# Kernel optimization log

Hardware: AMD Instinct MI355X
Metric: run time of the kernel (lower is better)

Reference implementation:

```python
import jax, jax.numpy as jnp
import numpy as np

B, IN, OUT = 2048, 64, 2048


def setup_inputs() -> dict:
    key = jax.random.key(0)
    k1, k2, k3 = jax.random.split(key, 3)
    x = jax.random.normal(k1, (B, IN), dtype=jnp.float32)
    # learned params (shapes per init: means [in, out], inv_std_dev [out, in, in])
    means = jax.random.uniform(k2, (IN, OUT), dtype=jnp.float32)
    # roughly like the inverse of a diagonal step matrix plus small noise
    inv_std_dev = (jax.random.normal(k3, (OUT, IN, IN), dtype=jnp.float32) * 0.05
                   + jnp.eye(IN, dtype=jnp.float32) * 0.5)
    return {"x": x, "means": means, "inv_std_dev": inv_std_dev}


def reference(x, means, inv_std_dev):
    # diff[b, o, i] = x[b, i] - means[i, o]   -> [B, OUT, IN]
    d = x[:, None, :] - means.T[None, :, :]
    # torch uses inv_std_dev.pow(2) (elementwise square), not a matrix square
    A = inv_std_dev * inv_std_dev  # [OUT, IN, IN]
    # per-neuron quadratic form: q[b, o] = d[b,o,:] @ A[o] @ d[b,o,:]
    q = jnp.einsum('boi,oij,boj->bo', d, A, d)
    return jnp.exp(-0.5 * q)  # [B, OUT]
```

## Files before the change

### kernel.cpp

```cpp
#include <hip/hip_runtime.h>
#include <hip/hip_bf16.h>

typedef __bf16 bf16x8 __attribute__((ext_vector_type(8)));
typedef float f32x4 __attribute__((ext_vector_type(4)));
typedef float f32x16 __attribute__((ext_vector_type(16)));

#define B_N 2048
#define O_N 2048
#define K_N 64

__device__ __forceinline__ void gld16(const void* g, void* l) {
    __builtin_amdgcn_global_load_lds(
        (const __attribute__((address_space(1))) void*)g,
        (__attribute__((address_space(3))) void*)l,
        16, 0, 0);
}

__global__ __launch_bounds__(256) void rbf_prep(
    const float* __restrict__ inv, const float* __restrict__ means,
    __bf16* __restrict__ Atp, __bf16* __restrict__ cPhi,
    __bf16* __restrict__ cPlo, float* __restrict__ kArr)
{
    __shared__ float s[64 * 65];
    __shared__ float mld[64];
    __shared__ float uw[128];
    const int o = blockIdx.x;
    const int t = threadIdx.x;
    const float4* src = (const float4*)(inv + (size_t)o * 4096);
#pragma unroll
    for (int k = 0; k < 4; ++k) {
        const int idx = k * 256 + t;
        const float4 v = src[idx];
        const int i = idx >> 4;
        const int j0 = (idx & 15) * 4;
        s[i * 65 + j0 + 0] = v.x * v.x;
        s[i * 65 + j0 + 1] = v.y * v.y;
        s[i * 65 + j0 + 2] = v.z * v.z;
        s[i * 65 + j0 + 3] = v.w * v.w;
    }
    if (t < 64) mld[t] = means[(size_t)t * O_N + o];
    __syncthreads();
    if (t < 64) {
        float u = 0.f;
#pragma unroll
        for (int i = 0; i < 64; ++i) u = fmaf(s[i * 65 + t], mld[i], u);
        uw[t] = u;
    } else if (t < 128) {
        const int j = t - 64;
        float w = 0.f;
#pragma unroll
        for (int i = 0; i < 64; ++i) w = fmaf(s[j * 65 + i], mld[i], w);
        uw[64 + j] = w;
    }
    __syncthreads();
    if (t < 64) {
        const float c = -(uw[t] + uw[64 + t]);
        const __bf16 hi = (__bf16)c;
        const __bf16 lo = (__bf16)(c - (float)hi);
        const size_t eidx = (size_t)(o >> 5) * 2048 + (size_t)(t >> 4) * 512
                          + (size_t)(o & 31) * 16 + (t & 15);
        cPhi[eidx] = hi;
        cPlo[eidx] = lo;
    }
    if (t == 0) {
        float kk = 0.f;
#pragma unroll
        for (int j = 0; j < 64; ++j) kk = fmaf(uw[j], mld[j], kk);
        kArr[o] = kk;
    }
#pragma unroll
    for (int r = 0; r < 2; ++r) {
        const int ch = r * 256 + t;
        const int ss = ch >> 7;
        const int j = (ch >> 1) & 63;
        const int hh = ch & 1;
        bf16x8 v;
#pragma unroll
        for (int e = 0; e < 8; ++e)
            v[e] = (__bf16)s[(16 * ss + 8 * hh + e) * 65 + j];
        *(bf16x8*)(Atp + (size_t)o * 4096 + (size_t)ch * 8) = v;
    }
}

__global__ __launch_bounds__(256, 2) void rbf_main(
    const float* __restrict__ x, const __bf16* __restrict__ Atp,
    const __bf16* __restrict__ cPhi, const __bf16* __restrict__ cPlo,
    const float* __restrict__ kArr, float* __restrict__ out)
{
    __shared__ __align__(16) __bf16 sA[3][4096];
    __shared__ __align__(16) float sLin[4][32][64];
    __shared__ float sK[32];

    const int tid = threadIdx.x;
    const int wave = tid >> 6;
    const int lane = tid & 63;
    const int b = lane & 31;
    const int h = lane >> 5;

    const int wg = (int)blockIdx.x;
    const int xcd = wg & 7;
    const int loc = wg >> 3;
    const int og = xcd * 8 + (loc >> 3);
    const int bg = loc & 7;
    const int oBase = og * 32;
    const int rowW = bg * 256 + wave * 64;

    const float* xr0 = x + (size_t)(rowW + b) * K_N;
    const float* xr1 = x + (size_t)(rowW + 32 + b) * K_N;

    const f32x16 zz = {0.f,0.f,0.f,0.f,0.f,0.f,0.f,0.f,
                       0.f,0.f,0.f,0.f,0.f,0.f,0.f,0.f};

    bf16x8 xh[2][4];
    f32x4 xd[2][2][4];
    {
        bf16x8 xl[2][4];
#pragma unroll
        for (int t = 0; t < 2; ++t) {
            const float* xr = t ? xr1 : xr0;
#pragma unroll
            for (int ss = 0; ss < 4; ++ss) {
                const float* p = xr + ss * 16 + h * 8;
                bf16x8 vh, vl;
#pragma unroll
                for (int e = 0; e < 8; ++e) {
                    const float v = p[e];
                    const __bf16 hi = (__bf16)v;
                    vh[e] = hi;
                    vl[e] = (__bf16)(v - (float)hi);
                }
                xh[t][ss] = vh; xl[t][ss] = vl;
            }
#pragma unroll
            for (int mt = 0; mt < 2; ++mt)
#pragma unroll
                for (int rq = 0; rq < 4; ++rq)
                    xd[t][mt][rq] = *(const f32x4*)(xr + mt * 32 + rq * 8 + h * 4);
        }
        const __bf16* chp = cPhi + (size_t)og * 2048;
        const __bf16* clp = cPlo + (size_t)og * 2048;
        bf16x8 fh[4], fl[4];
#pragma unroll
        for (int ss = 0; ss < 4; ++ss) {
            fh[ss] = *(const bf16x8*)(chp + ss * 512 + b * 16 + h * 8);
            fl[ss] = *(const bf16x8*)(clp + ss * 512 + b * 16 + h * 8);
        }
#pragma unroll
        for (int t = 0; t < 2; ++t) {
            f32x16 lin = zz;
#pragma unroll
            for (int ss = 0; ss < 4; ++ss) {
                lin = __builtin_amdgcn_mfma_f32_32x32x16_bf16(fh[ss], xh[t][ss], lin, 0, 0, 0);
                lin = __builtin_amdgcn_mfma_f32_32x32x16_bf16(fh[ss], xl[t][ss], lin, 0, 0, 0);
                lin = __builtin_amdgcn_mfma_f32_32x32x16_bf16(fl[ss], xh[t][ss], lin, 0, 0, 0);
            }
#pragma unroll
            for (int r = 0; r < 16; ++r)
                sLin[wave][(r & 3) + 8 * (r >> 2) + 4 * h][t * 32 + b] = lin[r];
        }
    }
    if (tid < 32) sK[tid] = kArr[oBase + tid];
    __syncthreads();

    const int L0 = tid * 16, L1 = 4096 + tid * 16;
    const int S0 = L0 ^ (((L0 >> 7) & 7) << 4);
    const int S1 = L1 ^ (((L1 >> 7) & 7) << 4);
    const char* gp = (const char*)(Atp + (size_t)oBase * 4096);
    gld16(gp + S0, (char*)&sA[0][0] + L0);
    gld16(gp + S1, (char*)&sA[0][0] + L1);
    gld16(gp + 8192 + S0, (char*)&sA[1][0] + L0);
    gld16(gp + 8192 + S1, (char*)&sA[1][0] + L1);

    const int off0 = (b * 32 + h * 16) ^ (((b >> 2) & 7) << 4);
    float* o0 = out + (size_t)(rowW + b) * O_N + oBase;
    float* o1 = out + (size_t)(rowW + 32 + b) * O_N + oBase;

    auto body = [&](int i, const __bf16* bufp) {
        __builtin_amdgcn_s_setprio(1);
        f32x16 a00 = zz, a01 = zz, a10 = zz, a11 = zz;
#pragma unroll
        for (int ss = 0; ss < 4; ++ss) {
            const char* base = (const char*)bufp + ss * 2048;
            const bf16x8 f0 = *(const bf16x8*)(base + off0);
            const bf16x8 f1 = *(const bf16x8*)(base + 1024 + off0);
            a00 = __builtin_amdgcn_mfma_f32_32x32x16_bf16(f0, xh[0][ss], a00, 0, 0, 0);
            a10 = __builtin_amdgcn_mfma_f32_32x32x16_bf16(f0, xh[1][ss], a10, 0, 0, 0);
            a01 = __builtin_amdgcn_mfma_f32_32x32x16_bf16(f1, xh[0][ss], a01, 0, 0, 0);
            a11 = __builtin_amdgcn_mfma_f32_32x32x16_bf16(f1, xh[1][ss], a11, 0, 0, 0);
        }
        __builtin_amdgcn_s_setprio(0);
        const float kk = sK[i];
        {
            float p0 = 0.f, p1 = 0.f, p2 = 0.f, p3 = 0.f;
#pragma unroll
            for (int e = 0; e < 4; ++e) {
                p0 = fmaf(a00[e],      xd[0][0][0][e], p0);
                p1 = fmaf(a00[4 + e],  xd[0][0][1][e], p1);
                p2 = fmaf(a00[8 + e],  xd[0][0][2][e], p2);
                p3 = fmaf(a00[12 + e], xd[0][0][3][e], p3);
                p0 = fmaf(a01[e],      xd[0][1][0][e], p0);
                p1 = fmaf(a01[4 + e],  xd[0][1][1][e], p1);
                p2 = fmaf(a01[8 + e],  xd[0][1][2][e], p2);
                p3 = fmaf(a01[12 + e], xd[0][1][3][e], p3);
            }
            float q = (p0 + p1) + (p2 + p3);
            q += __shfl_xor(q, 32, 64);
            q += sLin[wave][i][b] + kk;
            const float ev = exp2f(q * -0.72134752044448170368f);
            if (h == 0) o0[i] = ev;
        }
        {
            float p0 = 0.f, p1 = 0.f, p2 = 0.f, p3 = 0.f;
#pragma unroll
            for (int e = 0; e < 4; ++e) {
                p0 = fmaf(a10[e],      xd[1][0][0][e], p0);
                p1 = fmaf(a10[4 + e],  xd[1][0][1][e], p1);
                p2 = fmaf(a10[8 + e],  xd[1][0][2][e], p2);
                p3 = fmaf(a10[12 + e], xd[1][0][3][e], p3);
                p0 = fmaf(a11[e],      xd[1][1][0][e], p0);
                p1 = fmaf(a11[4 + e],  xd[1][1][1][e], p1);
                p2 = fmaf(a11[8 + e],  xd[1][1][2][e], p2);
                p3 = fmaf(a11[12 + e], xd[1][1][3][e], p3);
            }
            float q = (p0 + p1) + (p2 + p3);
            q += __shfl_xor(q, 32, 64);
            q += sLin[wave][i][32 + b] + kk;
            const float ev = exp2f(q * -0.72134752044448170368f);
            if (h == 0) o1[i] = ev;
        }
    };

#define RBF_ITER(I, BR, BW, WAIT) do {                                   \
    __builtin_amdgcn_s_barrier();          \
    __builtin_amdgcn_sched_barrier(0);                                   \
    { const int pf_ = ((I) + 2 <= 31) ? ((I) + 2) : 31;                  \
      const char* gn_ = gp + (size_t)pf_ * 8192;                         \
      gld16(gn_ + S0, (char*)&sA[(BW)][0] + L0);                         \
      gld16(gn_ + S1, (char*)&sA[(BW)][0] + L1); }                       \
    asm volatile("s_waitcnt " WAIT ::: "memory");                        \
    __builtin_amdgcn_s_barrier();              \
    __builtin_amdgcn_sched_barrier(0);                                   \
    body((I), (const __bf16*)&sA[(BR)][0]);                              \
} while (0)

    RBF_ITER(0, 0, 2, "vmcnt(4)");
    RBF_ITER(1, 1, 0, "vmcnt(6)");
#pragma unroll 1
    for (int ii = 0; ii < 10; ++ii) {
        const int i = 2 + ii * 3;
        RBF_ITER(i,     2, 1, "vmcnt(8)");
        RBF_ITER(i + 1, 0, 2, "vmcnt(8)");
        RBF_ITER(i + 2, 1, 0, "vmcnt(8)");
    }
#undef RBF_ITER
}

extern "C" void kernel_launch(void* const* d_in, const int* in_sizes, int n_in,
                              void* d_out, int out_size, void* d_ws, size_t ws_size,
                              hipStream_t stream)
{
    const float* x = (const float*)d_in[0];
    const float* means = (const float*)d_in[1];
    const float* inv = (const float*)d_in[2];
    float* out = (float*)d_out;

    char* w = (char*)d_ws;
    __bf16* Atp  = (__bf16*)w;
    __bf16* cPhi = (__bf16*)(w + (size_t)O_N * 4096 * 2);
    __bf16* cPlo = (__bf16*)(w + (size_t)O_N * 4096 * 2 + 262144);
    float*  kArr = (float*)(w + (size_t)O_N * 4096 * 2 + 524288);

    rbf_prep<<<dim3(O_N), dim3(256), 0, stream>>>(inv, means, Atp, cPhi, cPlo, kArr);
    rbf_main<<<dim3(512), dim3(256), 0, stream>>>(x, Atp, cPhi, cPlo, kArr, out);

    (void)in_sizes; (void)n_in; (void)out_size; (void)ws_size;
}
```

Before: 64.07 us.

## Halve output tile per block, double-buffer A, and vectorize output stores

Each block now handles 16 output neurons instead of 32, so the grid doubles to 1024 blocks. Launch bounds rise to 4 blocks per SIMD, and the shared-memory footprint shrinks because the A buffer goes from triple to double buffering. The hand-scheduled pipeline with explicit vmcnt waits is replaced by a simple loop using __syncthreads, which trades explicit overlap control for higher occupancy. Output writes are gathered into 4-float vectors per lane instead of scattered scalar stores. The linear-term MFMA still computes 32 columns and discards half, which adds redundant work.

```diff
diff --git a/kernel.cpp b/kernel.cpp
--- a/kernel.cpp
+++ b/kernel.cpp
@@ -82,14 +82,14 @@
     }
 }
 
-__global__ __launch_bounds__(256, 2) void rbf_main(
+__global__ __launch_bounds__(256, 4) void rbf_main(
     const float* __restrict__ x, const __bf16* __restrict__ Atp,
     const __bf16* __restrict__ cPhi, const __bf16* __restrict__ cPlo,
     const float* __restrict__ kArr, float* __restrict__ out)
 {
-    __shared__ __align__(16) __bf16 sA[3][4096];
-    __shared__ __align__(16) float sLin[4][32][64];
-    __shared__ float sK[32];
+    __shared__ __align__(16) __bf16 sA[2][4096];
+    __shared__ __align__(16) float sLin[4][16][64];
+    __shared__ float sK[16];
 
     const int tid = threadIdx.x;
     const int wave = tid >> 6;
@@ -100,9 +100,9 @@
     const int wg = (int)blockIdx.x;
     const int xcd = wg & 7;
     const int loc = wg >> 3;
-    const int og = xcd * 8 + (loc >> 3);
+    const int og = xcd * 16 + (loc >> 3);
     const int bg = loc & 7;
-    const int oBase = og * 32;
+    const int oBase = og * 16;
     const int rowW = bg * 256 + wave * 64;
 
     const float* xr0 = x + (size_t)(rowW + b) * K_N;
@@ -137,8 +137,10 @@
                 for (int rq = 0; rq < 4; ++rq)
                     xd[t][mt][rq] = *(const f32x4*)(xr + mt * 32 + rq * 8 + h * 4);
         }
-        const __bf16* chp = cPhi + (size_t)og * 2048;
-        const __bf16* clp = cPlo + (size_t)og * 2048;
+        const int og32 = og >> 1;
+        const int sel = og & 1;
+        const __bf16* chp = cPhi + (size_t)og32 * 2048;
+        const __bf16* clp = cPlo + (size_t)og32 * 2048;
         bf16x8 fh[4], fl[4];
 #pragma unroll
         for (int ss = 0; ss < 4; ++ss) {
@@ -154,13 +156,18 @@
                 lin = __builtin_amdgcn_mfma_f32_32x32x16_bf16(fh[ss], xl[t][ss], lin, 0, 0, 0);
                 lin = __builtin_amdgcn_mfma_f32_32x32x16_bf16(fl[ss], xh[t][ss], lin, 0, 0, 0);
             }
-#pragma unroll
-            for (int r = 0; r < 16; ++r)
-                sLin[wave][(r & 3) + 8 * (r >> 2) + 4 * h][t * 32 + b] = lin[r];
-        }
-    }
-    if (tid < 32) sK[tid] = kArr[oBase + tid];
-    __syncthreads();
+            if (sel == 0) {
+#pragma unroll
+                for (int r = 0; r < 8; ++r)
+                    sLin[wave][(r & 3) + 8 * (r >> 2) + 4 * h][t * 32 + b] = lin[r];
+            } else {
+#pragma unroll
+                for (int r = 8; r < 16; ++r)
+                    sLin[wave][(r & 3) + 8 * (r >> 2) + 4 * h - 16][t * 32 + b] = lin[r];
+            }
+        }
+    }
+    if (tid < 16) sK[tid] = kArr[oBase + tid];
 
     const int L0 = tid * 16, L1 = 4096 + tid * 16;
     const int S0 = L0 ^ (((L0 >> 7) & 7) << 4);
@@ -168,19 +175,27 @@
     const char* gp = (const char*)(Atp + (size_t)oBase * 4096);
     gld16(gp + S0, (char*)&sA[0][0] + L0);
     gld16(gp + S1, (char*)&sA[0][0] + L1);
-    gld16(gp + 8192 + S0, (char*)&sA[1][0] + L0);
-    gld16(gp + 8192 + S1, (char*)&sA[1][0] + L1);
 
     const int off0 = (b * 32 + h * 16) ^ (((b >> 2) & 7) << 4);
-    float* o0 = out + (size_t)(rowW + b) * O_N + oBase;
-    float* o1 = out + (size_t)(rowW + 32 + b) * O_N + oBase;
-
-    auto body = [&](int i, const __bf16* bufp) {
+    float* outp = out + (size_t)(rowW + lane) * O_N + oBase;
+
+    float q4[4];
+#pragma unroll 4
+    for (int i = 0; i < 16; ++i) {
+        __syncthreads();
+        if (i < 15) {
+            const char* gn = gp + (size_t)(i + 1) * 8192;
+            char* ld = (char*)&sA[(i + 1) & 1][0];
+            gld16(gn + S0, ld + L0);
+            gld16(gn + S1, ld + L1);
+        }
+        const char* bufp = (const char*)&sA[i & 1][0];
+
         __builtin_amdgcn_s_setprio(1);
         f32x16 a00 = zz, a01 = zz, a10 = zz, a11 = zz;
 #pragma unroll
         for (int ss = 0; ss < 4; ++ss) {
-            const char* base = (const char*)bufp + ss * 2048;
+            const char* base = bufp + ss * 2048;
             const bf16x8 f0 = *(const bf16x8*)(base + off0);
             const bf16x8 f1 = *(const bf16x8*)(base + 1024 + off0);
             a00 = __builtin_amdgcn_mfma_f32_32x32x16_bf16(f0, xh[0][ss], a00, 0, 0, 0);
@@ -189,7 +204,9 @@
             a11 = __builtin_amdgcn_mfma_f32_32x32x16_bf16(f1, xh[1][ss], a11, 0, 0, 0);
         }
         __builtin_amdgcn_s_setprio(0);
+
         const float kk = sK[i];
+        float ev0, ev1;
         {
             float p0 = 0.f, p1 = 0.f, p2 = 0.f, p3 = 0.f;
 #pragma unroll
@@ -206,8 +223,7 @@
             float q = (p0 + p1) + (p2 + p3);
             q += __shfl_xor(q, 32, 64);
             q += sLin[wave][i][b] + kk;
-            const float ev = exp2f(q * -0.72134752044448170368f);
-            if (h == 0) o0[i] = ev;
+            ev0 = exp2f(q * -0.72134752044448170368f);
         }
         {
             float p0 = 0.f, p1 = 0.f, p2 = 0.f, p3 = 0.f;
@@ -225,34 +241,15 @@
             float q = (p0 + p1) + (p2 + p3);
             q += __shfl_xor(q, 32, 64);
             q += sLin[wave][i][32 + b] + kk;
-            const float ev = exp2f(q * -0.72134752044448170368f);
-            if (h == 0) o1[i] = ev;
-        }
-    };
-
-#define RBF_ITER(I, BR, BW, WAIT) do {                                   \
-    __builtin_amdgcn_s_barrier();          \
-    __builtin_amdgcn_sched_barrier(0);                                   \
-    { const int pf_ = ((I) + 2 <= 31) ? ((I) + 2) : 31;                  \
-      const char* gn_ = gp + (size_t)pf_ * 8192;                         \
-      gld16(gn_ + S0, (char*)&sA[(BW)][0] + L0);                         \
-      gld16(gn_ + S1, (char*)&sA[(BW)][0] + L1); }                       \
-    asm volatile("s_waitcnt " WAIT ::: "memory");                        \
-    __builtin_amdgcn_s_barrier();              \
-    __builtin_amdgcn_sched_barrier(0);                                   \
-    body((I), (const __bf16*)&sA[(BR)][0]);                              \
-} while (0)
-
-    RBF_ITER(0, 0, 2, "vmcnt(4)");
-    RBF_ITER(1, 1, 0, "vmcnt(6)");
-#pragma unroll 1
-    for (int ii = 0; ii < 10; ++ii) {
-        const int i = 2 + ii * 3;
-        RBF_ITER(i,     2, 1, "vmcnt(8)");
-        RBF_ITER(i + 1, 0, 2, "vmcnt(8)");
-        RBF_ITER(i + 2, 1, 0, "vmcnt(8)");
-    }
-#undef RBF_ITER
+            ev1 = exp2f(q * -0.72134752044448170368f);
+        }
+        q4[i & 3] = h ? ev1 : ev0;
+
+        if ((i & 3) == 3) {
+            const f32x4 v = {q4[0], q4[1], q4[2], q4[3]};
+            *(f32x4*)(outp + (i - 3)) = v;
+        }
+    }
 }
 
 extern "C" void kernel_launch(void* const* d_in, const int* in_sizes, int n_in,
@@ -271,7 +268,7 @@
     float*  kArr = (float*)(w + (size_t)O_N * 4096 * 2 + 524288);
 
     rbf_prep<<<dim3(O_N), dim3(256), 0, stream>>>(inv, means, Atp, cPhi, cPlo, kArr);
-    rbf_main<<<dim3(512), dim3(256), 0, stream>>>(x, Atp, cPhi, cPlo, kArr, out);
+    rbf_main<<<dim3(1024), dim3(256), 0, stream>>>(x, Atp, cPhi, cPlo, kArr, out);
 
     (void)in_sizes; (void)n_in; (void)out_size; (void)ws_size;
 }
```

Result: slower. 243.4 us (+279.9%).
